# Kernel tuning notes

Hardware: AMD Instinct MI355X
Metric: run time of the kernel (lower is better)

## Reference

```python
import jax, jax.numpy as jnp
import numpy as np

FEATS = [(100, 100), (50, 50), (25, 25), (13, 13)]  # (W, H) per level
BS, NQ, D = 2, 10000, 256
NH, NL, NP, G = 8, 4, 4, 8
HD = D // NH


def grid_sample_bilinear(im, grid):
    """torch.nn.functional.grid_sample(mode='bilinear', padding_mode='zeros', align_corners=False).
    im: [N, C, H, W]; grid: [N, Hg, Wg, 2] in [-1, 1] (x, y). Returns [N, C, Hg, Wg]."""
    N, C, H, W = im.shape
    Hg, Wg = grid.shape[1], grid.shape[2]
    x = (grid[..., 0] + 1.0) * (W * 0.5) - 0.5
    y = (grid[..., 1] + 1.0) * (H * 0.5) - 0.5
    x0 = jnp.floor(x); y0 = jnp.floor(y)
    wx1 = x - x0; wx0 = 1.0 - wx1
    wy1 = y - y0; wy0 = 1.0 - wy1
    imf = im.reshape(N, C, H * W)

    def corner(xi, yi, w):
        inb = (xi >= 0) & (xi < W) & (yi >= 0) & (yi < H)
        xi_c = jnp.clip(xi, 0, W - 1).astype(jnp.int32)
        yi_c = jnp.clip(yi, 0, H - 1).astype(jnp.int32)
        idx = (yi_c * W + xi_c).reshape(N, 1, Hg * Wg)
        vals = jnp.take_along_axis(imf, idx, axis=2).reshape(N, C, Hg, Wg)
        return vals * (w * inb.astype(im.dtype))[:, None]

    out = (corner(x0, y0, wx0 * wy0) + corner(x0 + 1, y0, wx1 * wy0)
           + corner(x0, y0 + 1, wx0 * wy1) + corner(x0 + 1, y0 + 1, wx1 * wy1))
    return out


def setup_inputs() -> dict:
    key = jax.random.key(0)
    ks = jax.random.split(key, 7)
    nv = sum(w * h for (w, h) in FEATS)
    return {
        "query": jax.random.normal(ks[0], (BS, NQ, D), jnp.float32),
        "value": jax.random.normal(ks[1], (BS, nv, NH, HD), jnp.float32),
        "reference_points": jax.random.uniform(ks[2], (BS, NQ, NL, 2), jnp.float32),
        "spatial_shapes": jnp.array(FEATS, jnp.float32),  # rows are (W, H)
        "W_off": jax.random.normal(ks[3], (NH * NL * NP * 2, D), jnp.float32) * 0.02,
        "b_off": jax.random.normal(ks[4], (NH * NL * NP * 2,), jnp.float32) * 0.5,
        "W_attn": jax.random.normal(ks[5], (NH * NL * NP, D), jnp.float32) * 0.02,
        "b_attn": jax.random.normal(ks[6], (NH * NL * NP,), jnp.float32) * 0.02,
    }


def reference(query, value, reference_points, spatial_shapes, W_off, b_off, W_attn, b_attn):
    bs, nq, _ = query.shape
    # sampling offsets: [bs, nq, NH, NL*NP*2] with (level, point, xy) layout
    off = (jnp.einsum('bqd,od->bqo', query, W_off) + b_off).reshape(bs, nq, NH, NL * NP * 2)
    # reference points tiled to the same (level, point, xy) layout
    ref = jnp.broadcast_to(reference_points[:, :, None, :, None, :],
                           (bs, nq, NH, NL, NP, 2)).reshape(bs, nq, NH, NL * NP * 2)
    # offset normalizer: (1/W, 1/H) per level, tiled over points
    inv = 1.0 / spatial_shapes  # [NL, 2]
    norm = jnp.broadcast_to(inv[:, None, :], (NL, NP, 2)).reshape(-1)
    loc = (ref + off * norm) * 2.0 - 1.0  # [bs, nq, NH, NL*NP*2]
    loc = loc.reshape(bs, nq, NH, NL, NP, 2)

    # attention weights: softmax over (NL*NP), then rearranged to [bs*NH, 1, nq/G, NL*G*NP]
    aw = jax.nn.softmax((jnp.einsum('bqd,od->bqo', query, W_attn) + b_attn)
                        .reshape(bs, nq, NH, NL * NP), axis=-1)
    aw = aw.reshape(bs, nq // G, G, NH, NL, NP).transpose(0, 3, 1, 4, 2, 5)
    aw = aw.reshape(bs * NH, 1, nq // G, NL * G * NP)

    # per-level grid_sample
    sizes = [w * h for (w, h) in FEATS]
    starts = np.concatenate([[0], np.cumsum(sizes)]).tolist()
    sampled = []
    for lvl, (Wl, Hl) in enumerate(FEATS):
        val_l = value[:, starts[lvl]:starts[lvl + 1]]  # [bs, Hl*Wl, NH, HD]
        val_l = val_l.transpose(0, 2, 3, 1).reshape(bs * NH, HD, Hl, Wl)
        grid_l = loc[:, :, :, lvl].transpose(0, 2, 1, 3, 4)  # [bs, NH, nq, NP, 2]
        grid_l = grid_l.reshape(bs * NH, nq // G, G * NP, 2)
        sampled.append(grid_sample_bilinear(val_l, grid_l))  # [bs*NH, HD, nq/G, G*NP]
    sv = jnp.concatenate(sampled, axis=-1)  # [bs*NH, HD, nq/G, NL*G*NP]

    out = sv * aw
    # reduce_sum linear (fixed 0/1 weight from init_weights) == sum over levels and points per group slot
    out = out.reshape(bs * NH, HD, nq // G, NL, G, NP).sum(axis=(3, 5))  # [bs*NH, HD, nq/G, G]
    return out.reshape(bs, NH * HD, nq)
```

## Files before the change

### kernel.cpp

```cpp
#include <hip/hip_runtime.h>

#define NQ   10000
#define BSZ  2
#define DIM  256
#define NH   8
#define HD   32
#define NLV  4
#define NPT  4
#define NV   13294
#define MT   (BSZ*NQ)
#define NOUT 384

typedef float  floatx4 __attribute__((ext_vector_type(4)));
typedef int    intx4   __attribute__((ext_vector_type(4)));
typedef __bf16 bf16x8  __attribute__((ext_vector_type(8)));

__device__ __forceinline__ unsigned short f32_to_bf16(float f) {
  unsigned int u = __float_as_uint(f);
  u += 0x7FFFu + ((u >> 16) & 1u);
  return (unsigned short)(u >> 16);
}

__global__ __launch_bounds__(256) void gemm_kernel(
    const float* __restrict__ query, const float* __restrict__ W_off,
    const float* __restrict__ W_attn,
    const float* __restrict__ b_off, const float* __restrict__ b_attn,
    float* __restrict__ raw) {
  __shared__ unsigned short As[64][40];
  __shared__ unsigned short Bs[128][40];
  const int n0 = blockIdx.x * 128;
  const int m0 = blockIdx.y * 64;
  const int tid  = threadIdx.x;
  const int wave = tid >> 6;
  const int lane = tid & 63;
  const int quad = lane >> 4;
  const int l16  = lane & 15;
  floatx4 acc[8] = {};
  const int ar = tid >> 2;
  const int ac = (tid & 3) * 8;
  const int br = tid >> 1;
  const int bc = (tid & 1) * 16;
  const float* __restrict__ Wsrc =
      (n0 < 256) ? (W_off + (size_t)n0 * DIM) : (W_attn + (size_t)(n0 - 256) * DIM);

  for (int k0 = 0; k0 < DIM; k0 += 32) {
    {
      int gm = m0 + ar;
      floatx4 a0 = {}, a1 = {};
      if (gm < MT) {
        const float* src = query + (size_t)gm * DIM + k0 + ac;
        a0 = *(const floatx4*)src;
        a1 = *(const floatx4*)(src + 4);
      }
      unsigned short t[8];
      t[0]=f32_to_bf16(a0.x); t[1]=f32_to_bf16(a0.y); t[2]=f32_to_bf16(a0.z); t[3]=f32_to_bf16(a0.w);
      t[4]=f32_to_bf16(a1.x); t[5]=f32_to_bf16(a1.y); t[6]=f32_to_bf16(a1.z); t[7]=f32_to_bf16(a1.w);
      *(uint4*)&As[ar][ac] = *(const uint4*)t;
    }
    {
      const float* src = Wsrc + (size_t)br * DIM + k0 + bc;
      floatx4 b0 = *(const floatx4*)src;
      floatx4 b1 = *(const floatx4*)(src + 4);
      floatx4 b2 = *(const floatx4*)(src + 8);
      floatx4 b3 = *(const floatx4*)(src + 12);
      unsigned short t[16];
      t[0]=f32_to_bf16(b0.x);  t[1]=f32_to_bf16(b0.y);  t[2]=f32_to_bf16(b0.z);  t[3]=f32_to_bf16(b0.w);
      t[4]=f32_to_bf16(b1.x);  t[5]=f32_to_bf16(b1.y);  t[6]=f32_to_bf16(b1.z);  t[7]=f32_to_bf16(b1.w);
      t[8]=f32_to_bf16(b2.x);  t[9]=f32_to_bf16(b2.y);  t[10]=f32_to_bf16(b2.z); t[11]=f32_to_bf16(b2.w);
      t[12]=f32_to_bf16(b3.x); t[13]=f32_to_bf16(b3.y); t[14]=f32_to_bf16(b3.z); t[15]=f32_to_bf16(b3.w);
      *(uint4*)&Bs[br][bc]     = *(const uint4*)t;
      *(uint4*)&Bs[br][bc + 8] = *(const uint4*)(t + 8);
    }
    __syncthreads();
    bf16x8 a = *(const bf16x8*)&As[wave*16 + l16][quad*8];
    #pragma unroll
    for (int nt = 0; nt < 8; nt++) {
      bf16x8 b = *(const bf16x8*)&Bs[nt*16 + l16][quad*8];
      acc[nt] = __builtin_amdgcn_mfma_f32_16x16x32_bf16(a, b, acc[nt], 0, 0, 0);
    }
    __syncthreads();
  }
  #pragma unroll
  for (int nt = 0; nt < 8; nt++) {
    int gn = n0 + nt*16 + l16;
    float bias = (gn < 256) ? b_off[gn] : b_attn[gn - 256];
    #pragma unroll
    for (int r = 0; r < 4; r++) {
      int gm = m0 + wave*16 + quad*4 + r;
      if (gm < MT) raw[(size_t)gm*NOUT + gn] = acc[nt][r] + bias;
    }
  }
}

__global__ __launch_bounds__(256) void sample_kernel(
    const float* __restrict__ raw, const float* __restrict__ value,
    const float* __restrict__ refp, float* __restrict__ out) {
  const int b  = blockIdx.y;
  const int q0 = blockIdx.x * 4;
  const int mbase = b * NQ + q0;
  const int tid = threadIdx.x;

  __shared__ union {
    struct { float px[512]; float py[512]; float logit[512]; } a;
    float outbuf[1120];
  } u;
  __shared__ int s_tab[4 * 8 * 132];

  const int WLI[4] = {100, 50, 25, 13};
  const int STI[4] = {0, 10000, 12500, 13125};

  #pragma unroll
  for (int it = 0; it < 2; ++it) {
    int slot = it * 256 + tid;
    int ql = slot >> 7, r = slot & 127, h = r >> 4, lp = r & 15, l = lp >> 2, p = lp & 3;
    int m = mbase + ql;
    const float* rp = raw + (size_t)m * NOUT;
    float offx = rp[h*32 + l*8 + p*2 + 0];
    float offy = rp[h*32 + l*8 + p*2 + 1];
    u.a.logit[slot] = rp[256 + h*16 + lp];
    float Wl = (float)WLI[l];
    float rx = refp[(m*NLV + l)*2 + 0];
    float ry = refp[(m*NLV + l)*2 + 1];
    u.a.px[slot] = rx * Wl + offx - 0.5f;
    u.a.py[slot] = ry * Wl + offy - 0.5f;
  }
  __syncthreads();

  if (tid < 32) {
    int base = tid * 16;
    float mx = -1e30f;
    #pragma unroll
    for (int i = 0; i < 16; i++) mx = fmaxf(mx, u.a.logit[base + i]);
    float s = 0.f;
    float e[16];
    #pragma unroll
    for (int i = 0; i < 16; i++) { e[i] = expf(u.a.logit[base + i] - mx); s += e[i]; }
    float inv = 1.f / s;
    #pragma unroll
    for (int i = 0; i < 16; i++) u.a.logit[base + i] = e[i] * inv;
  }
  __syncthreads();

  #pragma unroll
  for (int it = 0; it < 2; ++it) {
    int slot = it * 256 + tid;
    int ql = slot >> 7, r = slot & 127, h = r >> 4, lp = r & 15, l = lp >> 2;
    float px = u.a.px[slot], py = u.a.py[slot], aw = u.a.logit[slot];
    float x0f = floorf(px), y0f = floorf(py);
    int x0 = (int)x0f, y0 = (int)y0f;
    float wx1 = px - x0f, wx0 = 1.f - wx1;
    float wy1 = py - y0f, wy0 = 1.f - wy1;
    int Wl = WLI[l], STl = STI[l];
    int row = (ql*8 + h) * 132 + lp * 8;
    #pragma unroll
    for (int t = 0; t < 4; ++t) {
      int xi = x0 + (t & 1), yi = y0 + (t >> 1);
      bool inb = (xi >= 0) & (xi < Wl) & (yi >= 0) & (yi < Wl);
      int off = inb ? ((STl + yi*Wl + xi) * 1024 + h * 128) : 0;
      float w = inb ? (aw * ((t & 1) ? wx1 : wx0) * ((t >> 1) ? wy1 : wy0)) : 0.f;
      s_tab[row + t]     = off;
      s_tab[row + 4 + t] = __float_as_int(w);
    }
  }
  __syncthreads();

  {
    const int ql = tid >> 6, lane = tid & 63, h = lane >> 3, cq = lane & 7;
    const char* vb = (const char*)value + (size_t)b * (NV*NH*HD*4) + cq * 16;
    floatx4 acc = {0.f, 0.f, 0.f, 0.f};
    const int rbase = (ql*8 + h) * 132;
    #pragma unroll 4
    for (int pt = 0; pt < 16; ++pt) {
      intx4   offs = *(const intx4*)  &s_tab[rbase + pt*8];
      floatx4 ws   = *(const floatx4*)&s_tab[rbase + pt*8 + 4];
      floatx4 v0 = *(const floatx4*)(vb + offs.x);
      floatx4 v1 = *(const floatx4*)(vb + offs.y);
      floatx4 v2 = *(const floatx4*)(vb + offs.z);
      floatx4 v3 = *(const floatx4*)(vb + offs.w);
      acc += ws.x * v0;
      acc += ws.y * v1;
      acc += ws.z * v2;
      acc += ws.w * v3;
    }
    int obase = ql*280 + h*33 + cq*4;
    u.outbuf[obase + 0] = acc.x;
    u.outbuf[obase + 1] = acc.y;
    u.outbuf[obase + 2] = acc.z;
    u.outbuf[obase + 3] = acc.w;
  }
  __syncthreads();

  {
    const int ch = tid, h = ch >> 5, c = ch & 31;
    floatx4 o;
    o.x = u.outbuf[0*280 + h*33 + c];
    o.y = u.outbuf[1*280 + h*33 + c];
    o.z = u.outbuf[2*280 + h*33 + c];
    o.w = u.outbuf[3*280 + h*33 + c];
    *(floatx4*)&out[((size_t)(b*DIM + ch))*NQ + q0] = o;
  }
}

extern "C" void kernel_launch(void* const* d_in, const int* in_sizes, int n_in,
                              void* d_out, int out_size, void* d_ws, size_t ws_size,
                              hipStream_t stream) {
  const float* query  = (const float*)d_in[0];
  const float* value  = (const float*)d_in[1];
  const float* refp   = (const float*)d_in[2];
  const float* W_off  = (const float*)d_in[4];
  const float* b_off  = (const float*)d_in[5];
  const float* W_attn = (const float*)d_in[6];
  const float* b_attn = (const float*)d_in[7];
  float* out = (float*)d_out;

  float* raw = (float*)d_ws;

  hipLaunchKernelGGL(gemm_kernel, dim3(3, 313), dim3(256), 0, stream,
                     query, W_off, W_attn, b_off, b_attn, raw);
  hipLaunchKernelGGL(sample_kernel, dim3(NQ / 4, BSZ), dim3(256), 0, stream,
                     raw, value, refp, out);
}
```

Before: 187.4 us.

## Write sampled output query-major to scratch and transpose in separate kernel

The sampling kernel now writes each query's 256 channels contiguously to a scratch buffer, replacing the LDS staging and the strided 16-byte stores into the channel-major output. A new tiled transpose kernel then converts the scratch buffer to the required [bs, C, nq] layout with coalesced reads and writes. Pixel coordinates are kept in registers instead of shared memory, and the attention logits get a padded shared layout, which cuts LDS use and one barrier. The cost is an extra kernel launch plus an additional round trip of about 20 MB through global memory.

```diff
diff --git a/kernel.cpp b/kernel.cpp
--- a/kernel.cpp
+++ b/kernel.cpp
@@ -94,20 +94,19 @@
 
 __global__ __launch_bounds__(256) void sample_kernel(
     const float* __restrict__ raw, const float* __restrict__ value,
-    const float* __restrict__ refp, float* __restrict__ out) {
+    const float* __restrict__ refp, float* __restrict__ tmp) {
   const int b  = blockIdx.y;
   const int q0 = blockIdx.x * 4;
   const int mbase = b * NQ + q0;
   const int tid = threadIdx.x;
 
-  __shared__ union {
-    struct { float px[512]; float py[512]; float logit[512]; } a;
-    float outbuf[1120];
-  } u;
-  __shared__ int s_tab[4 * 8 * 132];
+  __shared__ int   s_tab[4 * 8 * 132];
+  __shared__ float s_aw[544];
 
   const int WLI[4] = {100, 50, 25, 13};
   const int STI[4] = {0, 10000, 12500, 13125};
+
+  float rpx[2], rpy[2];
 
   #pragma unroll
   for (int it = 0; it < 2; ++it) {
@@ -117,27 +116,27 @@
     const float* rp = raw + (size_t)m * NOUT;
     float offx = rp[h*32 + l*8 + p*2 + 0];
     float offy = rp[h*32 + l*8 + p*2 + 1];
-    u.a.logit[slot] = rp[256 + h*16 + lp];
+    s_aw[(ql*8 + h)*17 + lp] = rp[256 + h*16 + lp];
     float Wl = (float)WLI[l];
     float rx = refp[(m*NLV + l)*2 + 0];
     float ry = refp[(m*NLV + l)*2 + 1];
-    u.a.px[slot] = rx * Wl + offx - 0.5f;
-    u.a.py[slot] = ry * Wl + offy - 0.5f;
+    rpx[it] = rx * Wl + offx - 0.5f;
+    rpy[it] = ry * Wl + offy - 0.5f;
   }
   __syncthreads();
 
   if (tid < 32) {
-    int base = tid * 16;
+    int base = tid * 17;
     float mx = -1e30f;
     #pragma unroll
-    for (int i = 0; i < 16; i++) mx = fmaxf(mx, u.a.logit[base + i]);
+    for (int i = 0; i < 16; i++) mx = fmaxf(mx, s_aw[base + i]);
     float s = 0.f;
     float e[16];
     #pragma unroll
-    for (int i = 0; i < 16; i++) { e[i] = expf(u.a.logit[base + i] - mx); s += e[i]; }
+    for (int i = 0; i < 16; i++) { e[i] = expf(s_aw[base + i] - mx); s += e[i]; }
     float inv = 1.f / s;
     #pragma unroll
-    for (int i = 0; i < 16; i++) u.a.logit[base + i] = e[i] * inv;
+    for (int i = 0; i < 16; i++) s_aw[base + i] = e[i] * inv;
   }
   __syncthreads();
 
@@ -145,7 +144,8 @@
   for (int it = 0; it < 2; ++it) {
     int slot = it * 256 + tid;
     int ql = slot >> 7, r = slot & 127, h = r >> 4, lp = r & 15, l = lp >> 2;
-    float px = u.a.px[slot], py = u.a.py[slot], aw = u.a.logit[slot];
+    float aw = s_aw[(ql*8 + h)*17 + lp];
+    float px = rpx[it], py = rpy[it];
     float x0f = floorf(px), y0f = floorf(py);
     int x0 = (int)x0f, y0 = (int)y0f;
     float wx1 = px - x0f, wx0 = 1.f - wx1;
@@ -164,40 +164,46 @@
   }
   __syncthreads();
 
-  {
-    const int ql = tid >> 6, lane = tid & 63, h = lane >> 3, cq = lane & 7;
-    const char* vb = (const char*)value + (size_t)b * (NV*NH*HD*4) + cq * 16;
-    floatx4 acc = {0.f, 0.f, 0.f, 0.f};
-    const int rbase = (ql*8 + h) * 132;
-    #pragma unroll 4
-    for (int pt = 0; pt < 16; ++pt) {
-      intx4   offs = *(const intx4*)  &s_tab[rbase + pt*8];
-      floatx4 ws   = *(const floatx4*)&s_tab[rbase + pt*8 + 4];
-      floatx4 v0 = *(const floatx4*)(vb + offs.x);
-      floatx4 v1 = *(const floatx4*)(vb + offs.y);
-      floatx4 v2 = *(const floatx4*)(vb + offs.z);
-      floatx4 v3 = *(const floatx4*)(vb + offs.w);
-      acc += ws.x * v0;
-      acc += ws.y * v1;
-      acc += ws.z * v2;
-      acc += ws.w * v3;
-    }
-    int obase = ql*280 + h*33 + cq*4;
-    u.outbuf[obase + 0] = acc.x;
-    u.outbuf[obase + 1] = acc.y;
-    u.outbuf[obase + 2] = acc.z;
-    u.outbuf[obase + 3] = acc.w;
-  }
-  __syncthreads();
-
-  {
-    const int ch = tid, h = ch >> 5, c = ch & 31;
-    floatx4 o;
-    o.x = u.outbuf[0*280 + h*33 + c];
-    o.y = u.outbuf[1*280 + h*33 + c];
-    o.z = u.outbuf[2*280 + h*33 + c];
-    o.w = u.outbuf[3*280 + h*33 + c];
-    *(floatx4*)&out[((size_t)(b*DIM + ch))*NQ + q0] = o;
+  const int ql = tid >> 6, lane = tid & 63, h = lane >> 3, cq = lane & 7;
+  const char* vb = (const char*)value + (size_t)b * (NV*NH*HD*4) + cq * 16;
+  floatx4 acc = {0.f, 0.f, 0.f, 0.f};
+  const int rbase = (ql*8 + h) * 132;
+  #pragma unroll 4
+  for (int pt = 0; pt < 16; ++pt) {
+    intx4   offs = *(const intx4*)  &s_tab[rbase + pt*8];
+    floatx4 ws   = *(const floatx4*)&s_tab[rbase + pt*8 + 4];
+    floatx4 v0 = *(const floatx4*)(vb + offs.x);
+    floatx4 v1 = *(const floatx4*)(vb + offs.y);
+    floatx4 v2 = *(const floatx4*)(vb + offs.z);
+    floatx4 v3 = *(const floatx4*)(vb + offs.w);
+    acc += ws.x * v0;
+    acc += ws.y * v1;
+    acc += ws.z * v2;
+    acc += ws.w * v3;
+  }
+  int m = mbase + ql;
+  *(floatx4*)&tmp[(size_t)m * DIM + h*HD + cq*4] = acc;
+}
+
+__global__ __launch_bounds__(256) void transpose_kernel(
+    const float* __restrict__ tmp, float* __restrict__ out) {
+  __shared__ float tile[32][33];
+  const int b  = blockIdx.z;
+  const int q0 = blockIdx.x * 32;
+  const int c0 = blockIdx.y * 32;
+  const int tx = threadIdx.x & 31;
+  const int ty = threadIdx.x >> 5;
+  #pragma unroll
+  for (int i = 0; i < 4; i++) {
+    int qq = q0 + ty + i*8;
+    tile[ty + i*8][tx] = (qq < NQ) ? tmp[((long)b*NQ + qq)*DIM + c0 + tx] : 0.f;
+  }
+  __syncthreads();
+  if (q0 + tx < NQ) {
+    #pragma unroll
+    for (int i = 0; i < 4; i++) {
+      out[((long)b*DIM + c0 + ty + i*8)*NQ + q0 + tx] = tile[tx][ty + i*8];
+    }
   }
 }
 
@@ -213,10 +219,14 @@
   const float* b_attn = (const float*)d_in[7];
   float* out = (float*)d_out;
 
-  float* raw = (float*)d_ws;
+  char* ws = (char*)d_ws;
+  float* raw = (float*)ws;
+  float* tmp = (float*)(ws + 30720000);
 
   hipLaunchKernelGGL(gemm_kernel, dim3(3, 313), dim3(256), 0, stream,
                      query, W_off, W_attn, b_off, b_attn, raw);
   hipLaunchKernelGGL(sample_kernel, dim3(NQ / 4, BSZ), dim3(256), 0, stream,
-                     raw, value, refp, out);
-}
+                     raw, value, refp, tmp);
+  hipLaunchKernelGGL(transpose_kernel, dim3(313, 8, 2), dim3(256), 0, stream,
+                     tmp, out);
+}
```

Measured after the change: 178.5 us. 1.05x faster.
